# Optimization experiments

Measured on AMD Instinct MI355X. Metric: run time of the kernel, lower is better.

Reference implementation:

```python
import jax, jax.numpy as jnp
import numpy as np
from jax import lax

H = 1024
NH = 16
R = 32
B, S = 32, 1024
LN_EPS = 1e-5

def _gelu(x):
    return jax.nn.gelu(x, approximate=False)

def setup_inputs() -> dict:
    key = jax.random.key(0)
    ks = jax.random.split(key, 24)
    w = lambda k, shape: jax.random.normal(k, shape, jnp.float32) * 0.02
    d = {}
    d['computation_results'] = jax.random.normal(ks[0], (B, S, H), jnp.float32)
    d['max_steps'] = 16
    # rule selector: Linear(H,H), GELU, Linear(H,R)
    d['rule_w1'] = w(ks[1], (H, H)); d['rule_b1'] = jnp.zeros((H,))
    d['rule_w2'] = w(ks[2], (R, H)); d['rule_b2'] = jnp.zeros((R,))
    d['rule_emb'] = jax.random.normal(ks[3], (R, H), jnp.float32)
    # MultiheadAttention packed in-proj [3H,H] and out-proj [H,H]
    d['attn_in_w'] = w(ks[4], (3 * H, H)); d['attn_in_b'] = jnp.zeros((3 * H,))
    d['attn_out_w'] = w(ks[5], (H, H)); d['attn_out_b'] = jnp.zeros((H,))
    # 2-layer LSTM, PyTorch gate order i,f,g,o
    d['lstm_wih0'] = w(ks[6], (4 * H, H)); d['lstm_whh0'] = w(ks[7], (4 * H, H))
    d['lstm_bih0'] = jnp.zeros((4 * H,)); d['lstm_bhh0'] = jnp.zeros((4 * H,))
    d['lstm_wih1'] = w(ks[8], (4 * H, H)); d['lstm_whh1'] = w(ks[9], (4 * H, H))
    d['lstm_bih1'] = jnp.zeros((4 * H,)); d['lstm_bhh1'] = jnp.zeros((4 * H,))
    # step generator: Linear(H,2H), LayerNorm(2H), GELU, Linear(2H,H)
    d['gen_w1'] = w(ks[10], (2 * H, H)); d['gen_b1'] = jnp.zeros((2 * H,))
    d['gen_ln_g'] = jnp.ones((2 * H,)); d['gen_ln_b'] = jnp.zeros((2 * H,))
    d['gen_w2'] = w(ks[11], (H, 2 * H)); d['gen_b2'] = jnp.zeros((H,))
    # step validator: Linear(2H,H), GELU, Linear(H,1), Sigmoid
    d['val_w1'] = w(ks[12], (H, 2 * H)); d['val_b1'] = jnp.zeros((H,))
    d['val_w2'] = w(ks[13], (1, H)); d['val_b2'] = jnp.zeros((1,))
    # proof verifier: Linear(H,H), GELU, Linear(H,1), Sigmoid
    d['ver_w1'] = w(ks[14], (H, H)); d['ver_b1'] = jnp.zeros((H,))
    d['ver_w2'] = w(ks[15], (1, H)); d['ver_b2'] = jnp.zeros((1,))
    return d


def reference(computation_results, max_steps, rule_w1, rule_b1, rule_w2, rule_b2, rule_emb,
              attn_in_w, attn_in_b, attn_out_w, attn_out_b,
              lstm_wih0, lstm_whh0, lstm_bih0, lstm_bhh0,
              lstm_wih1, lstm_whh1, lstm_bih1, lstm_bhh1,
              gen_w1, gen_b1, gen_ln_g, gen_ln_b, gen_w2, gen_b2,
              val_w1, val_b1, val_w2, val_b2,
              ver_w1, ver_b1, ver_w2, ver_b2):
    comp = computation_results
    b, s, h = comp.shape
    dh = h // NH
    scale = dh ** -0.5
    wq, wk, wv = jnp.split(attn_in_w, 3, axis=0)
    bq, bk, bv = jnp.split(attn_in_b, 3, axis=0)
    # K/V projections of the static context, computed once outside the step loop
    K = (comp @ wk.T + bk).reshape(b, s, NH, dh)  # [B,S,NH,dh]
    V = (comp @ wv.T + bv).reshape(b, s, NH, dh)
    lstm_params = ((lstm_wih0, lstm_whh0, lstm_bih0, lstm_bhh0),
                   (lstm_wih1, lstm_whh1, lstm_bih1, lstm_bhh1))

    def step(carry, _):
        ps, hmem, cmem = carry  # ps: [B,H]; hmem/cmem: [2,B,H]
        # rule selection
        logits = _gelu(ps @ rule_w1.T + rule_b1) @ rule_w2.T + rule_b2
        probs = jax.nn.softmax(logits, axis=-1)  # [B,R]
        sel = probs @ rule_emb  # [B,H]
        # single-query multi-head attention over computation context
        q = (ps @ wq.T + bq).reshape(b, NH, dh) * scale
        scores = jnp.einsum('bhd,bshd->bhs', q, K)
        a = jax.nn.softmax(scores, axis=-1)  # [B,NH,S]
        ctx = jnp.einsum('bhs,bshd->bhd', a, V).reshape(b, h) @ attn_out_w.T + attn_out_b
        attn_avg = a.mean(axis=1)  # head-averaged weights, [B,S]
        # 2-layer LSTM cell, one timestep
        x = ps
        hs, cs = [], []
        for l, (wih, whh, bih, bhh) in enumerate(lstm_params):
            g = x @ wih.T + bih + hmem[l] @ whh.T + bhh
            gi, gf, gg, go = jnp.split(g, 4, axis=-1)
            cn = jax.nn.sigmoid(gf) * cmem[l] + jax.nn.sigmoid(gi) * jnp.tanh(gg)
            hn = jax.nn.sigmoid(go) * jnp.tanh(cn)
            hs.append(hn); cs.append(cn); x = hn
        mem_out = x
        # step generator with LayerNorm+GELU
        si = ps + sel + ctx + mem_out
        z = si @ gen_w1.T + gen_b1
        mu = z.mean(axis=-1, keepdims=True)
        var = ((z - mu) ** 2).mean(axis=-1, keepdims=True)
        z = (z - mu) / jnp.sqrt(var + LN_EPS) * gen_ln_g + gen_ln_b
        nxt = _gelu(z) @ gen_w2.T + gen_b2
        val = jax.nn.sigmoid(_gelu(jnp.concatenate([ps, nxt], axis=-1) @ val_w1.T + val_b1) @ val_w2.T + val_b2)
        return (nxt, jnp.stack(hs), jnp.stack(cs)), (nxt, probs, val, attn_avg)

    init_state = comp[:, 0, :]
    carry0 = (init_state, jnp.zeros((2, b, h), comp.dtype), jnp.zeros((2, b, h), comp.dtype))
    (final, _, _), (steps, probs, vals, attn) = lax.scan(step, carry0, None, length=int(max_steps))
    proof_steps = jnp.concatenate([init_state[None], steps], axis=0)  # [T+1,B,H]
    proof_validity = jax.nn.sigmoid(_gelu(final @ ver_w1.T + ver_b1) @ ver_w2.T + ver_b2)  # [B,1]
    return proof_steps, proof_validity, probs, vals, attn
```

## Files before the change

kernel.cpp:

```cpp
#include <hip/hip_runtime.h>

typedef unsigned short u16;
typedef unsigned int u32;
typedef __attribute__((ext_vector_type(8))) short short8v;
typedef __attribute__((ext_vector_type(4))) float f32x4;

#define MFMA16(a,b,c) __builtin_amdgcn_mfma_f32_16x16x32_bf16((a),(b),(c),0,0,0)

__device__ __forceinline__ u16 f2bf(float f){
  u32 u = __float_as_uint(f);
  return (u16)((u + 0x7fffu + ((u >> 16) & 1u)) >> 16);
}
__device__ __forceinline__ float bf2f(u16 h){ return __uint_as_float(((u32)h) << 16); }
__device__ __forceinline__ float gelu_f(float x){ return 0.5f * x * (1.f + erff(x * 0.70710678118654752f)); }
__device__ __forceinline__ float sigm_f(float x){ return 1.f / (1.f + __expf(-x)); }
__device__ __forceinline__ void acc4(float4& a, const float4 b){ a.x+=b.x; a.y+=b.y; a.z+=b.z; a.w+=b.w; }

__device__ __forceinline__ void gl16(const void* g, void* l){
  __builtin_amdgcn_global_load_lds((const __attribute__((address_space(1))) u32*)g,
                                   (__attribute__((address_space(3))) u32*)l, 16, 0, 0);
}

struct CastJobs { const float* s[13]; u16* d[13]; int start[14]; };
__global__ __launch_bounds__(256) void cast_all_k(CastJobs J){
  int bx = blockIdx.x, j = 0;
  #pragma unroll
  for (int t = 0; t < 13; t++) if (bx >= J.start[t + 1]) j = t + 1;
  int i = (bx - J.start[j]) * 1024 + threadIdx.x * 4;
  float4 v = *(const float4*)(J.s[j] + i);
  ushort4 o; o.x = f2bf(v.x); o.y = f2bf(v.y); o.z = f2bf(v.z); o.w = f2bf(v.w);
  *(ushort4*)(J.d[j] + i) = o;
}

__global__ __launch_bounds__(256) void cast_k(const float* __restrict__ s, u16* __restrict__ d, int n){
  int i = (blockIdx.x * 256 + threadIdx.x) * 4;
  if (i + 3 < n){
    float4 v = *(const float4*)(s + i);
    ushort4 o; o.x = f2bf(v.x); o.y = f2bf(v.y); o.z = f2bf(v.z); o.w = f2bf(v.w);
    *(ushort4*)(d + i) = o;
  }
}

__global__ __launch_bounds__(256) void init_k(const float* __restrict__ comp, float* ps0, float* outp,
                                              float* h0, float* c0, float* h1, float* c1){
  int i = blockIdx.x * 256 + threadIdx.x;
  int b = i >> 10, hh = i & 1023;
  float v = comp[(size_t)b * 1048576 + hh];
  ps0[i] = v; outp[i] = v;
  h0[i] = 0.f; c0[i] = 0.f; h1[i] = 0.f; c1[i] = 0.f;
}

__global__ __launch_bounds__(256) void gemmkv_k(const u16* __restrict__ compb,
    const u16* __restrict__ Wk, const u16* __restrict__ Wv,
    const float* __restrict__ bk, const float* __restrict__ bv,
    u16* __restrict__ Kt, u16* __restrict__ Vb)
{
  __shared__ u16 As[128 * 32];
  __shared__ u16 Bs[128 * 32];
  int tid = threadIdx.x;
  const u16 *msrc, *nsrc;
  int m0, n0, isK = (blockIdx.z != 0);
  if (!isK){ m0 = blockIdx.x * 128; n0 = blockIdx.y * 128; msrc = compb; nsrc = Wv; }
  else     { m0 = blockIdx.y * 128; n0 = blockIdx.x * 128; msrc = Wk;    nsrc = compb; }

  int w = tid >> 6, l = tid & 63, lr = l & 15, lk = l >> 4;
  int wm = (w >> 1) * 64, wn = (w & 1) * 64;
  f32x4 acc[4][4];
  #pragma unroll
  for (int i = 0; i < 4; i++)
    #pragma unroll
    for (int j = 0; j < 4; j++) acc[i][j] = (f32x4){0.f,0.f,0.f,0.f};

  int row0 = tid >> 2, k80 = (tid & 3) * 8;
  for (int kc = 0; kc < 1024; kc += 32){
    #pragma unroll
    for (int r = 0; r < 2; r++){
      int i = tid + r * 256;
      int row = row0 + r * 64, k8 = k80;
      gl16(msrc + (size_t)(m0 + row) * 1024 + kc + k8, As + i * 8);
      gl16(nsrc + (size_t)(n0 + row) * 1024 + kc + k8, Bs + i * 8);
    }
    __syncthreads();
    short8v a[4], bb[4];
    #pragma unroll
    for (int mi = 0; mi < 4; mi++) a[mi]  = *(const short8v*)(As + (wm + mi * 16 + lr) * 32 + lk * 8);
    #pragma unroll
    for (int ni = 0; ni < 4; ni++) bb[ni] = *(const short8v*)(Bs + (wn + ni * 16 + lr) * 32 + lk * 8);
    #pragma unroll
    for (int mi = 0; mi < 4; mi++)
      #pragma unroll
      for (int ni = 0; ni < 4; ni++)
        acc[mi][ni] = MFMA16(a[mi], bb[ni], acc[mi][ni]);
    __syncthreads();
  }
  #pragma unroll
  for (int mi = 0; mi < 4; mi++)
    #pragma unroll
    for (int ni = 0; ni < 4; ni++)
      #pragma unroll
      for (int r = 0; r < 4; r++){
        int row = m0 + wm + mi * 16 + lk * 4 + r;
        int col = n0 + wn + ni * 16 + lr;
        if (!isK){
          Vb[(size_t)row * 1024 + col] = f2bf(acc[mi][ni][r] + bv[col]);
        } else {
          int b = col >> 10, s = col & 1023;
          Kt[((size_t)b * 1024 + row) * 1024 + s] = f2bf(acc[mi][ni][r] + bk[row]);
        }
      }
}

struct LinSeg {
  const float* X0; const float* Xa; const float* Xb; const float* Xc;
  const u16* W1; const float* b1;
  const float* Y; const u16* W2; const float* b2;
  float* out; float* out2;
  int K1, ld1, K2, ld2, N, act;
  float scale;
  float* stats;
  const float* lng; const float* lnb; const float* lnstats;
};

__device__ __forceinline__ short8v pack8(float4 v0, float4 v1){
  short8v r;
  r[0]=(short)f2bf(v0.x); r[1]=(short)f2bf(v0.y); r[2]=(short)f2bf(v0.z); r[3]=(short)f2bf(v0.w);
  r[4]=(short)f2bf(v1.x); r[5]=(short)f2bf(v1.y); r[6]=(short)f2bf(v1.z); r[7]=(short)f2bf(v1.w);
  return r;
}

__device__ __forceinline__ short8v load_sum8(const LinSeg& S, int row, int kb){
  size_t o = (size_t)row * S.K1 + kb;
  float4 v0 = *(const float4*)(S.X0 + o);
  float4 v1 = *(const float4*)(S.X0 + o + 4);
  if (S.lng){
    float mu = S.lnstats[row] * (1.f / 2048.f);
    float ms = S.lnstats[32 + row] * (1.f / 2048.f);
    float rstd = rsqrtf(ms - mu * mu + 1e-5f);
    float4 g0 = *(const float4*)(S.lng + kb), g1 = *(const float4*)(S.lng + kb + 4);
    float4 b0 = *(const float4*)(S.lnb + kb), b1 = *(const float4*)(S.lnb + kb + 4);
    v0.x = gelu_f((v0.x - mu) * rstd * g0.x + b0.x);
    v0.y = gelu_f((v0.y - mu) * rstd * g0.y + b0.y);
    v0.z = gelu_f((v0.z - mu) * rstd * g0.z + b0.z);
    v0.w = gelu_f((v0.w - mu) * rstd * g0.w + b0.w);
    v1.x = gelu_f((v1.x - mu) * rstd * g1.x + b1.x);
    v1.y = gelu_f((v1.y - mu) * rstd * g1.y + b1.y);
    v1.z = gelu_f((v1.z - mu) * rstd * g1.z + b1.z);
    v1.w = gelu_f((v1.w - mu) * rstd * g1.w + b1.w);
  } else {
    if (S.Xa){ acc4(v0, *(const float4*)(S.Xa + o)); acc4(v1, *(const float4*)(S.Xa + o + 4)); }
    if (S.Xb){ acc4(v0, *(const float4*)(S.Xb + o)); acc4(v1, *(const float4*)(S.Xb + o + 4)); }
    if (S.Xc){ acc4(v0, *(const float4*)(S.Xc + o)); acc4(v1, *(const float4*)(S.Xc + o + 4)); }
  }
  return pack8(v0, v1);
}
__device__ __forceinline__ short8v load_y8(const float* __restrict__ p){
  return pack8(*(const float4*)(p), *(const float4*)(p + 4));
}

typedef float Red32[32][32];

__device__ void lin_body(const LinSeg& S, int bi, int tid, Red32* red){
  int c0 = bi * 32;
  int w = tid >> 6, l = tid & 63, lr = l & 15, lk = l >> 4;
  f32x4 acc[2][2];
  #pragma unroll
  for (int i = 0; i < 2; i++)
    #pragma unroll
    for (int j = 0; j < 2; j++) acc[i][j] = (f32x4){0.f,0.f,0.f,0.f};

  {
    int chunk = S.K1 >> 3;
    int kb0 = w * chunk + lk * 8;
    for (int kk = 0; kk < chunk; kk += 32){
      int kb = kb0 + kk;
      short8v a0 = load_sum8(S, lr, kb);
      short8v a1 = load_sum8(S, lr + 16, kb);
      short8v w0 = *(const short8v*)(S.W1 + (size_t)(c0 + lr) * S.ld1 + kb);
      short8v w1 = *(const short8v*)(S.W1 + (size_t)(c0 + lr + 16) * S.ld1 + kb);
      acc[0][0] = MFMA16(a0, w0, acc[0][0]);
      acc[0][1] = MFMA16(a0, w1, acc[0][1]);
      acc[1][0] = MFMA16(a1, w0, acc[1][0]);
      acc[1][1] = MFMA16(a1, w1, acc[1][1]);
    }
  }
  if (S.Y){
    int chunk = S.K2 >> 3;
    int kb0 = w * chunk + lk * 8;
    for (int kk = 0; kk < chunk; kk += 32){
      int kb = kb0 + kk;
      short8v a0 = load_y8(S.Y + (size_t)lr * S.K2 + kb);
      short8v a1 = load_y8(S.Y + (size_t)(lr + 16) * S.K2 + kb);
      short8v w0 = *(const short8v*)(S.W2 + (size_t)(c0 + lr) * S.ld2 + kb);
      short8v w1 = *(const short8v*)(S.W2 + (size_t)(c0 + lr + 16) * S.ld2 + kb);
      acc[0][0] = MFMA16(a0, w0, acc[0][0]);
      acc[0][1] = MFMA16(a0, w1, acc[0][1]);
      acc[1][0] = MFMA16(a1, w0, acc[1][0]);
      acc[1][1] = MFMA16(a1, w1, acc[1][1]);
    }
  }
  #pragma unroll
  for (int mi = 0; mi < 2; mi++)
    #pragma unroll
    for (int ni = 0; ni < 2; ni++)
      #pragma unroll
      for (int r = 0; r < 4; r++)
        red[w][mi * 16 + lk * 4 + r][ni * 16 + lr] = acc[mi][ni][r];
  __syncthreads();
  float vout[2]; int iout[2];
  int cnt = 0;
  for (int i = tid; i < 1024; i += 512){
    int row = i >> 5, col = i & 31;
    float v = 0.f;
    #pragma unroll
    for (int ww = 0; ww < 8; ww++) v += red[ww][row][col];
    v += S.b1[c0 + col];
    if (S.b2) v += S.b2[c0 + col];
    if (S.act == 1) v = gelu_f(v);
    else if (S.act == 2) v *= S.scale;
    S.out[(size_t)row * S.N + c0 + col] = v;
    if (S.out2) S.out2[(size_t)row * S.N + c0 + col] = v;
    vout[cnt] = v; iout[cnt] = i; cnt++;
  }
  if (S.stats){
    __syncthreads();
    float* rf = (float*)red;
    rf[iout[0]] = vout[0]; rf[1024 + iout[0]] = vout[0] * vout[0];
    rf[iout[1]] = vout[1]; rf[1024 + iout[1]] = vout[1] * vout[1];
    __syncthreads();
    if (tid < 32){
      float s = 0.f, s2 = 0.f;
      #pragma unroll
      for (int cc = 0; cc < 32; cc++){ s += rf[tid * 32 + cc]; s2 += rf[1024 + tid * 32 + cc]; }
      atomicAdd(S.stats + tid, s);
      atomicAdd(S.stats + 32 + tid, s2);
    }
  }
}

__global__ __launch_bounds__(512) void linmulti_k(LinSeg s0, LinSeg s1, LinSeg s2, int n0, int n1){
  __shared__ float red[8][32][32];
  int bx = blockIdx.x, tid = threadIdx.x;
  if (bx < n0) lin_body(s0, bx, tid, red);
  else if (bx < n0 + n1) lin_body(s1, bx - n0, tid, red);
  else lin_body(s2, bx - n0 - n1, tid, red);
}

__global__ __launch_bounds__(512) void valver_k(const u16* __restrict__ vw1, const float* __restrict__ vb1,
    const u16* __restrict__ verw1, const float* __restrict__ verb1,
    const float* __restrict__ proof, float* __restrict__ v1){
  __shared__ float red[8][32][32];
  int t = blockIdx.y;
  LinSeg S = {};
  if (t < 16){
    S.X0 = proof + (size_t)t * 32768; S.K1 = 1024; S.W1 = vw1; S.ld1 = 2048; S.b1 = vb1;
    S.Y = proof + (size_t)(t + 1) * 32768; S.K2 = 1024; S.W2 = vw1 + 1024; S.ld2 = 2048;
  } else {
    S.X0 = proof + (size_t)16 * 32768; S.K1 = 1024; S.W1 = verw1; S.ld1 = 1024; S.b1 = verb1;
  }
  S.out = v1 + (size_t)t * 32768; S.N = 1024; S.act = 1;
  lin_body(S, blockIdx.x, threadIdx.x, red);
}

__global__ __launch_bounds__(256) void dotsig_b_k(const float* __restrict__ v1,
    const float* __restrict__ w2v, const float* __restrict__ b2v,
    const float* __restrict__ w2ver, const float* __restrict__ b2ver,
    float* __restrict__ out_vals, float* __restrict__ out_valid){
  int t = blockIdx.x;
  const float* w = (t < 16) ? w2v : w2ver;
  const float* bs = (t < 16) ? b2v : b2ver;
  const float* x = v1 + (size_t)t * 32768;
  int b = threadIdx.x >> 3, l8 = threadIdx.x & 7;
  const float* xr = x + (size_t)b * 1024;
  float acc = 0.f;
  #pragma unroll 8
  for (int kk = 0; kk < 32; kk++){
    int k = kk * 32 + l8 * 4;
    float4 xv = *(const float4*)(xr + k);
    float4 wv = *(const float4*)(w + k);
    acc += xv.x * wv.x + xv.y * wv.y + xv.z * wv.z + xv.w * wv.w;
  }
  acc += __shfl_xor(acc, 1); acc += __shfl_xor(acc, 2); acc += __shfl_xor(acc, 4);
  if (l8 == 0){
    float r = sigm_f(acc + bs[0]);
    if (t < 16) out_vals[t * 32 + b] = r; else out_valid[b] = r;
  }
}

__global__ __launch_bounds__(256) void attn_rg0_k(const float* __restrict__ q,
    const u16* __restrict__ Kt, const u16* __restrict__ Vb,
    float* __restrict__ afull, float* __restrict__ ctx0,
    const float* __restrict__ h1a, const float* __restrict__ w2, const float* __restrict__ b2,
    const float* __restrict__ emb, float* __restrict__ probs_out, float* __restrict__ sel,
    const float* __restrict__ g, const float* __restrict__ cprev,
    float* __restrict__ cn, float* __restrict__ hn)
{
  int tid = threadIdx.x;
  if (blockIdx.x >= 544){
    int idx = (blockIdx.x - 544) * 256 + tid;
    int b = idx >> 10, j = idx & 1023;
    const float* gr = g + (size_t)b * 4096;
    float gi = gr[j], gf = gr[1024 + j], gg = gr[2048 + j], go = gr[3072 + j];
    float c = sigm_f(gf) * cprev[idx] + sigm_f(gi) * tanhf(gg);
    cn[idx] = c;
    hn[idx] = sigm_f(go) * tanhf(c);
    return;
  }
  if (blockIdx.x >= 512){
    int b = blockIdx.x - 512;
    __shared__ float lg[32], pshared[32];
    int j = tid >> 3, l8 = tid & 7;
    const float* xr = h1a + b * 1024;
    const float* wr = w2 + j * 1024;
    float acc = 0.f;
    #pragma unroll 8
    for (int kk = 0; kk < 32; kk++){
      int k = kk * 32 + l8 * 4;
      float4 xv = *(const float4*)(xr + k);
      float4 wv = *(const float4*)(wr + k);
      acc += xv.x * wv.x + xv.y * wv.y + xv.z * wv.z + xv.w * wv.w;
    }
    acc += __shfl_xor(acc, 1); acc += __shfl_xor(acc, 2); acc += __shfl_xor(acc, 4);
    if (l8 == 0) lg[j] = acc + b2[j];
    __syncthreads();
    if (tid < 32){
      float v = lg[tid];
      float m = v;
      for (int o = 1; o < 32; o <<= 1) m = fmaxf(m, __shfl_xor(m, o));
      float e = __expf(v - m);
      float s = e;
      for (int o = 1; o < 32; o <<= 1) s += __shfl_xor(s, o);
      float p = e / s;
      pshared[tid] = p;
      probs_out[b * 32 + tid] = p;
    }
    __syncthreads();
    for (int j2 = tid; j2 < 1024; j2 += 256){
      float a2 = 0.f;
      #pragma unroll
      for (int r = 0; r < 32; r++) a2 += pshared[r] * emb[r * 1024 + j2];
      sel[b * 1024 + j2] = a2;
    }
    return;
  }
  int bh = blockIdx.x;
  int b = bh >> 4, h = bh & 15;
  __shared__ float qs[64];
  __shared__ float sc[1024];
  __shared__ float rmx[4], rsm[4];
  __shared__ float ctxp[8][64];
  if (tid < 64) qs[tid] = q[bh * 64 + tid];
  __syncthreads();
  const u32* kt = (const u32*)(Kt + (size_t)bh * 65536);
  float a0 = 0.f, a1 = 0.f, a2 = 0.f, a3 = 0.f;
  #pragma unroll 8
  for (int d = 0; d < 64; d++){
    float qd = qs[d];
    u32 p0 = kt[d * 512 + tid];
    u32 p1 = kt[d * 512 + tid + 256];
    a0 += qd * bf2f((u16)(p0 & 0xffff)); a1 += qd * bf2f((u16)(p0 >> 16));
    a2 += qd * bf2f((u16)(p1 & 0xffff)); a3 += qd * bf2f((u16)(p1 >> 16));
  }
  float mx = fmaxf(fmaxf(a0, a1), fmaxf(a2, a3));
  for (int o = 1; o < 64; o <<= 1) mx = fmaxf(mx, __shfl_xor(mx, o));
  if ((tid & 63) == 0) rmx[tid >> 6] = mx;
  __syncthreads();
  mx = fmaxf(fmaxf(rmx[0], rmx[1]), fmaxf(rmx[2], rmx[3]));
  float e0 = __expf(a0 - mx), e1 = __expf(a1 - mx), e2 = __expf(a2 - mx), e3 = __expf(a3 - mx);
  float sm = e0 + e1 + e2 + e3;
  for (int o = 1; o < 64; o <<= 1) sm += __shfl_xor(sm, o);
  if ((tid & 63) == 0) rsm[tid >> 6] = sm;
  __syncthreads();
  sm = rsm[0] + rsm[1] + rsm[2] + rsm[3];
  float inv = 1.f / sm;
  float* ar = afull + (size_t)bh * 1024;
  float2 w0 = make_float2(e0 * inv, e1 * inv);
  float2 w1 = make_float2(e2 * inv, e3 * inv);
  *(float2*)(sc + 2 * tid) = w0;       *(float2*)(ar + 2 * tid) = w0;
  *(float2*)(sc + 512 + 2 * tid) = w1; *(float2*)(ar + 512 + 2 * tid) = w1;
  __syncthreads();
  int d2 = (tid & 31) * 2, chunk = tid >> 5;
  const u16* vb = Vb + ((size_t)(b * 1024) * 16 + h) * 64 + d2;
  float c0 = 0.f, c1 = 0.f;
  for (int s = chunk * 128; s < chunk * 128 + 128; s++){
    u32 vv = *(const u32*)(vb + (size_t)s * 1024);
    float wv = sc[s];
    c0 += wv * bf2f((u16)(vv & 0xffff));
    c1 += wv * bf2f((u16)(vv >> 16));
  }
  *(float2*)&ctxp[chunk][d2] = make_float2(c0, c1);
  __syncthreads();
  if (tid < 64){
    float r = 0.f;
    #pragma unroll
    for (int c = 0; c < 8; c++) r += ctxp[c][tid];
    ctx0[bh * 64 + tid] = r;
  }
}

__global__ __launch_bounds__(256) void gz_k(const float* __restrict__ g, const float* __restrict__ cprev,
                                            float* __restrict__ cn, float* __restrict__ hn,
                                            float* __restrict__ stats){
  if (blockIdx.x == 0 && threadIdx.x < 64) stats[threadIdx.x] = 0.f;
  int idx = blockIdx.x * 256 + threadIdx.x;
  int b = idx >> 10, j = idx & 1023;
  const float* gr = g + (size_t)b * 4096;
  float gi = gr[j], gf = gr[1024 + j], gg = gr[2048 + j], go = gr[3072 + j];
  float c = sigm_f(gf) * cprev[idx] + sigm_f(gi) * tanhf(gg);
  cn[idx] = c;
  hn[idx] = sigm_f(go) * tanhf(c);
}

__global__ __launch_bounds__(256) void attnavg_all_k(const float* __restrict__ afull, float* __restrict__ out){
  int idx = blockIdx.x * 256 + threadIdx.x;
  int t = idx >> 15, r = idx & 32767;
  int b = r >> 10, s = r & 1023;
  const float* base = afull + (size_t)t * 524288 + (size_t)b * 16384;
  float acc = 0.f;
  #pragma unroll
  for (int h = 0; h < 16; h++) acc += base[h * 1024 + s];
  out[idx] = acc * (1.f / 16.f);
}

extern "C" void kernel_launch(void* const* d_in, const int* in_sizes, int n_in,
                              void* d_out, int out_size, void* d_ws, size_t ws_size,
                              hipStream_t stream) {
  const float* comp      = (const float*)d_in[0];
  const float* rule_w1   = (const float*)d_in[2];
  const float* rule_b1   = (const float*)d_in[3];
  const float* rule_w2   = (const float*)d_in[4];
  const float* rule_b2   = (const float*)d_in[5];
  const float* rule_emb  = (const float*)d_in[6];
  const float* attn_in_w = (const float*)d_in[7];
  const float* attn_in_b = (const float*)d_in[8];
  const float* attn_out_w= (const float*)d_in[9];
  const float* attn_out_b= (const float*)d_in[10];
  const float* wih0 = (const float*)d_in[11];
  const float* whh0 = (const float*)d_in[12];
  const float* bih0 = (const float*)d_in[13];
  const float* bhh0 = (const float*)d_in[14];
  const float* wih1 = (const float*)d_in[15];
  const float* whh1 = (const float*)d_in[16];
  const float* bih1 = (const float*)d_in[17];
  const float* bhh1 = (const float*)d_in[18];
  const float* gen_w1 = (const float*)d_in[19];
  const float* gen_b1 = (const float*)d_in[20];
  const float* ln_g   = (const float*)d_in[21];
  const float* ln_b   = (const float*)d_in[22];
  const float* gen_w2 = (const float*)d_in[23];
  const float* gen_b2 = (const float*)d_in[24];
  const float* val_w1 = (const float*)d_in[25];
  const float* val_b1 = (const float*)d_in[26];
  const float* val_w2 = (const float*)d_in[27];
  const float* val_b2 = (const float*)d_in[28];
  const float* ver_w1 = (const float*)d_in[29];
  const float* ver_b1 = (const float*)d_in[30];
  const float* ver_w2 = (const float*)d_in[31];
  const float* ver_b2 = (const float*)d_in[32];

  float* out_f     = (float*)d_out;
  float* out_proof = out_f;
  float* out_valid = out_f + 17 * 32768;
  float* out_probs = out_valid + 32;
  float* out_vals  = out_probs + 16 * 1024;
  float* out_attn  = out_vals + 16 * 32;

  char* wp = (char*)d_ws;
  auto carve = [&](size_t bytes) -> void* {
    void* p = (void*)wp; wp += (bytes + 255) & ~(size_t)255; return p;
  };
  u16* Kt    = (u16*)carve((size_t)33554432 * 2);
  u16* Vb    = (u16*)carve((size_t)33554432 * 2);
  u16* compb = (u16*)carve((size_t)33554432 * 2);
  float* afull_all = (float*)compb;
  u16* rw1b  = (u16*)carve(2097152);
  u16* wqb   = (u16*)carve(2097152);
  u16* wkb   = (u16*)carve(2097152);
  u16* wvb   = (u16*)carve(2097152);
  u16* aowb  = (u16*)carve(2097152);
  u16* wih0b = (u16*)carve(8388608);
  u16* whh0b = (u16*)carve(8388608);
  u16* wih1b = (u16*)carve(8388608);
  u16* whh1b = (u16*)carve(8388608);
  u16* gw1b  = (u16*)carve(4194304);
  u16* gw2b  = (u16*)carve(4194304);
  u16* vw1b  = (u16*)carve(4194304);
  u16* verw1b= (u16*)carve(2097152);
  float* psb[2]  = { (float*)carve(131072), (float*)carve(131072) };
  float* h0b[2]  = { (float*)carve(131072), (float*)carve(131072) };
  float* c0b[2]  = { (float*)carve(131072), (float*)carve(131072) };
  float* h1b[2]  = { (float*)carve(131072), (float*)carve(131072) };
  float* c1b[2]  = { (float*)carve(131072), (float*)carve(131072) };
  float* h1act = (float*)carve(131072);
  float* sel   = (float*)carve(131072);
  float* qbuf  = (float*)carve(131072);
  float* ctx0  = (float*)carve(131072);
  float* ctxb  = (float*)carve(131072);
  float* gbuf  = (float*)carve(524288);
  float* zbuf  = (float*)carve(262144);
  float* v1buf = (float*)carve(2228224);
  float* lnstats = (float*)carve(256);
  (void)ws_size; (void)in_sizes; (void)n_in; (void)out_size;

  CastJobs J;
  const float* srcs[13] = { rule_w1, attn_in_w, attn_in_w + 1048576, attn_in_w + 2097152,
                            attn_out_w, wih0, whh0, wih1, whh1, gen_w1, gen_w2, val_w1, ver_w1 };
  u16* dsts[13] = { rw1b, wqb, wkb, wvb, aowb, wih0b, whh0b, wih1b, whh1b, gw1b, gw2b, vw1b, verw1b };
  int sizes[13] = { 1048576, 1048576, 1048576, 1048576, 1048576,
                    4194304, 4194304, 4194304, 4194304, 2097152, 2097152, 2097152, 1048576 };
  int st = 0;
  for (int i = 0; i < 13; i++){ J.s[i] = srcs[i]; J.d[i] = dsts[i]; J.start[i] = st; st += sizes[i] / 1024; }
  J.start[13] = st;
  cast_all_k<<<dim3(st), dim3(256), 0, stream>>>(J);
  cast_k<<<dim3(32768), dim3(256), 0, stream>>>(comp, compb, 33554432);

  gemmkv_k<<<dim3(256, 8, 2), dim3(256), 0, stream>>>(compb, wkb, wvb,
      attn_in_b + 1024, attn_in_b + 2048, Kt, Vb);

  init_k<<<dim3(128), dim3(256), 0, stream>>>(comp, psb[0], out_proof,
      h0b[0], c0b[0], h1b[0], c1b[0]);

  auto mkseg = [&](const float* X0, const float* Xa, const float* Xb, const float* Xc,
                   int K1, const u16* W1, int ld1, const float* bb1,
                   const float* Y, int K2, const u16* W2, int ld2, const float* bb2,
                   float* out, int N, int act, float scl, float* out2) -> LinSeg {
    LinSeg S = {};
    S.X0 = X0; S.Xa = Xa; S.Xb = Xb; S.Xc = Xc; S.K1 = K1; S.W1 = W1; S.ld1 = ld1; S.b1 = bb1;
    S.Y = Y; S.K2 = K2; S.W2 = W2; S.ld2 = ld2; S.b2 = bb2;
    S.out = out; S.N = N; S.act = act; S.scale = scl; S.out2 = out2;
    return S;
  };
  auto lin1 = [&](LinSeg S){
    linmulti_k<<<dim3(S.N / 32), dim3(512), 0, stream>>>(S, S, S, S.N / 32, 0);
  };

  for (int t = 0; t < 16; t++){
    int cur = t & 1, nx = cur ^ 1;
    float* ps = psb[cur];
    float* afull_t = afull_all + (size_t)t * 524288;
    LinSeg sRule = mkseg(ps, 0, 0, 0, 1024, rw1b, 1024, rule_b1, 0, 0, 0, 0, 0, h1act, 1024, 1, 0.f, 0);
    LinSeg sQ    = mkseg(ps, 0, 0, 0, 1024, wqb, 1024, attn_in_b, 0, 0, 0, 0, 0, qbuf, 1024, 2, 0.125f, 0);
    LinSeg sL0   = mkseg(ps, 0, 0, 0, 1024, wih0b, 1024, bih0, h0b[cur], 1024, whh0b, 1024, bhh0,
                         gbuf, 4096, 0, 0.f, 0);
    linmulti_k<<<dim3(192), dim3(512), 0, stream>>>(sRule, sQ, sL0, 32, 32);
    attn_rg0_k<<<dim3(672), dim3(256), 0, stream>>>(qbuf, Kt, Vb, afull_t, ctx0,
        h1act, rule_w2, rule_b2, rule_emb, out_probs + t * 1024, sel,
        gbuf, c0b[cur], c0b[nx], h0b[nx]);
    LinSeg sCtx = mkseg(ctx0, 0, 0, 0, 1024, aowb, 1024, attn_out_b, 0, 0, 0, 0, 0, ctxb, 1024, 0, 0.f, 0);
    LinSeg sL1  = mkseg(h0b[nx], 0, 0, 0, 1024, wih1b, 1024, bih1, h1b[cur], 1024, whh1b, 1024, bhh1,
                        gbuf, 4096, 0, 0.f, 0);
    linmulti_k<<<dim3(160), dim3(512), 0, stream>>>(sCtx, sL1, sL1, 32, 128);
    gz_k<<<dim3(128), dim3(256), 0, stream>>>(gbuf, c1b[cur], c1b[nx], h1b[nx], lnstats);
    LinSeg sG1 = mkseg(ps, sel, ctxb, h1b[nx], 1024, gw1b, 1024, gen_b1, 0, 0, 0, 0, 0,
                       zbuf, 2048, 0, 0.f, 0);
    sG1.stats = lnstats;
    lin1(sG1);
    LinSeg sG2 = mkseg(zbuf, 0, 0, 0, 2048, gw2b, 2048, gen_b2, 0, 0, 0, 0, 0,
                       psb[nx], 1024, 0, 0.f, out_proof + (size_t)(t + 1) * 32768);
    sG2.lng = ln_g; sG2.lnb = ln_b; sG2.lnstats = lnstats;
    lin1(sG2);
  }
  valver_k<<<dim3(32, 17), dim3(512), 0, stream>>>(vw1b, val_b1, verw1b, ver_b1, out_proof, v1buf);
  dotsig_b_k<<<dim3(17), dim3(256), 0, stream>>>(v1buf, val_w2, val_b2, ver_w2, ver_b2,
      out_vals, out_valid);
  attnavg_all_k<<<dim3(2048), dim3(256), 0, stream>>>(afull_all, out_attn);
}
```

Measured before the change: 1.948 ms.

## Fuse LSTM cell update into gate GEMM epilogue and tile KV GEMM deeper

Each LSTM gate GEMM block now computes the i,f,g,o columns for 8 hidden units together. The cell and hidden update then runs in the reduction epilogue, which removes the gbuf round trip, the gz_k kernel and the LSTM tail of the attention kernel. The stats zeroing moves into linmulti_k. Separately, the K/V projection GEMM uses a K-chunk of 64 with XOR-swizzled LDS and an XCD-aware block remap for L2 locality. This adds extra per-block reduction work and stride-1024 weight row access in the gate path.

```diff
diff --git a/kernel.cpp b/kernel.cpp
--- a/kernel.cpp
+++ b/kernel.cpp
@@ -55,13 +55,17 @@
     const float* __restrict__ bk, const float* __restrict__ bv,
     u16* __restrict__ Kt, u16* __restrict__ Vb)
 {
-  __shared__ u16 As[128 * 32];
-  __shared__ u16 Bs[128 * 32];
+  __shared__ u16 As[128 * 64];
+  __shared__ u16 Bs[128 * 64];
   int tid = threadIdx.x;
-  const u16 *msrc, *nsrc;
-  int m0, n0, isK = (blockIdx.z != 0);
-  if (!isK){ m0 = blockIdx.x * 128; n0 = blockIdx.y * 128; msrc = compb; nsrc = Wv; }
-  else     { m0 = blockIdx.y * 128; n0 = blockIdx.x * 128; msrc = Wk;    nsrc = compb; }
+  int x = blockIdx.x;
+  int xcd = x & 7, p = x >> 3;
+  int cpanel = xcd * 32 + (p >> 3);
+  int wpanel = p & 7;
+  int isK = (blockIdx.z != 0);
+  const u16 *msrc, *nsrc; int m0, n0;
+  if (!isK){ m0 = cpanel * 128; n0 = wpanel * 128; msrc = compb; nsrc = Wv; }
+  else     { m0 = wpanel * 128; n0 = cpanel * 128; msrc = Wk;    nsrc = compb; }
 
   int w = tid >> 6, l = tid & 63, lr = l & 15, lk = l >> 4;
   int wm = (w >> 1) * 64, wn = (w & 1) * 64;
@@ -71,26 +75,37 @@
     #pragma unroll
     for (int j = 0; j < 4; j++) acc[i][j] = (f32x4){0.f,0.f,0.f,0.f};
 
-  int row0 = tid >> 2, k80 = (tid & 3) * 8;
-  for (int kc = 0; kc < 1024; kc += 32){
-    #pragma unroll
-    for (int r = 0; r < 2; r++){
-      int i = tid + r * 256;
-      int row = row0 + r * 64, k8 = k80;
-      gl16(msrc + (size_t)(m0 + row) * 1024 + kc + k8, As + i * 8);
-      gl16(nsrc + (size_t)(n0 + row) * 1024 + kc + k8, Bs + i * 8);
+  for (int kc = 0; kc < 1024; kc += 64){
+    #pragma unroll
+    for (int r = 0; r < 4; r++){
+      int s = tid + r * 256;
+      int row = s >> 3, pp = s & 7;
+      int lg = pp ^ (row & 7);
+      gl16(msrc + (size_t)(m0 + row) * 1024 + kc + lg * 8, As + s * 8);
+      gl16(nsrc + (size_t)(n0 + row) * 1024 + kc + lg * 8, Bs + s * 8);
     }
     __syncthreads();
-    short8v a[4], bb[4];
-    #pragma unroll
-    for (int mi = 0; mi < 4; mi++) a[mi]  = *(const short8v*)(As + (wm + mi * 16 + lr) * 32 + lk * 8);
-    #pragma unroll
-    for (int ni = 0; ni < 4; ni++) bb[ni] = *(const short8v*)(Bs + (wn + ni * 16 + lr) * 32 + lk * 8);
-    #pragma unroll
-    for (int mi = 0; mi < 4; mi++)
-      #pragma unroll
-      for (int ni = 0; ni < 4; ni++)
-        acc[mi][ni] = MFMA16(a[mi], bb[ni], acc[mi][ni]);
+    #pragma unroll
+    for (int kk = 0; kk < 2; kk++){
+      short8v a[4], bb[4];
+      #pragma unroll
+      for (int mi = 0; mi < 4; mi++){
+        int row = wm + mi * 16 + lr;
+        int ph = (kk * 4 + lk) ^ (row & 7);
+        a[mi] = *(const short8v*)(As + row * 64 + ph * 8);
+      }
+      #pragma unroll
+      for (int ni = 0; ni < 4; ni++){
+        int row = wn + ni * 16 + lr;
+        int ph = (kk * 4 + lk) ^ (row & 7);
+        bb[ni] = *(const short8v*)(Bs + row * 64 + ph * 8);
+      }
+      #pragma unroll
+      for (int mi = 0; mi < 4; mi++)
+        #pragma unroll
+        for (int ni = 0; ni < 4; ni++)
+          acc[mi][ni] = MFMA16(a[mi], bb[ni], acc[mi][ni]);
+    }
     __syncthreads();
   }
   #pragma unroll
@@ -115,10 +130,11 @@
   const u16* W1; const float* b1;
   const float* Y; const u16* W2; const float* b2;
   float* out; float* out2;
-  int K1, ld1, K2, ld2, N, act;
+  int K1, ld1, K2, ld2, N, act, gate;
   float scale;
   float* stats;
   const float* lng; const float* lnb; const float* lnstats;
+  const float* cprev; float* cout; float* hout;
 };
 
 __device__ __forceinline__ short8v pack8(float4 v0, float4 v1){
@@ -160,8 +176,10 @@
 typedef float Red32[32][32];
 
 __device__ void lin_body(const LinSeg& S, int bi, int tid, Red32* red){
-  int c0 = bi * 32;
+  int c0 = bi * 32, j0 = bi * 8;
   int w = tid >> 6, l = tid & 63, lr = l & 15, lk = l >> 4;
+  int wc0 = S.gate ? ((lr >> 3) << 10) + j0 + (lr & 7) : c0 + lr;
+  int wc1 = S.gate ? (((lr + 16) >> 3) << 10) + j0 + ((lr + 16) & 7) : c0 + lr + 16;
   f32x4 acc[2][2];
   #pragma unroll
   for (int i = 0; i < 2; i++)
@@ -175,8 +193,8 @@
       int kb = kb0 + kk;
       short8v a0 = load_sum8(S, lr, kb);
       short8v a1 = load_sum8(S, lr + 16, kb);
-      short8v w0 = *(const short8v*)(S.W1 + (size_t)(c0 + lr) * S.ld1 + kb);
-      short8v w1 = *(const short8v*)(S.W1 + (size_t)(c0 + lr + 16) * S.ld1 + kb);
+      short8v w0 = *(const short8v*)(S.W1 + (size_t)wc0 * S.ld1 + kb);
+      short8v w1 = *(const short8v*)(S.W1 + (size_t)wc1 * S.ld1 + kb);
       acc[0][0] = MFMA16(a0, w0, acc[0][0]);
       acc[0][1] = MFMA16(a0, w1, acc[0][1]);
       acc[1][0] = MFMA16(a1, w0, acc[1][0]);
@@ -190,8 +208,8 @@
       int kb = kb0 + kk;
       short8v a0 = load_y8(S.Y + (size_t)lr * S.K2 + kb);
       short8v a1 = load_y8(S.Y + (size_t)(lr + 16) * S.K2 + kb);
-      short8v w0 = *(const short8v*)(S.W2 + (size_t)(c0 + lr) * S.ld2 + kb);
-      short8v w1 = *(const short8v*)(S.W2 + (size_t)(c0 + lr + 16) * S.ld2 + kb);
+      short8v w0 = *(const short8v*)(S.W2 + (size_t)wc0 * S.ld2 + kb);
+      short8v w1 = *(const short8v*)(S.W2 + (size_t)wc1 * S.ld2 + kb);
       acc[0][0] = MFMA16(a0, w0, acc[0][0]);
       acc[0][1] = MFMA16(a0, w1, acc[0][1]);
       acc[1][0] = MFMA16(a1, w0, acc[1][0]);
@@ -206,6 +224,29 @@
       for (int r = 0; r < 4; r++)
         red[w][mi * 16 + lk * 4 + r][ni * 16 + lr] = acc[mi][ni][r];
   __syncthreads();
+  if (S.gate){
+    if (tid < 256){
+      int row = tid >> 3, j = tid & 7;
+      float s[4];
+      #pragma unroll
+      for (int g = 0; g < 4; g++){
+        float v = 0.f;
+        #pragma unroll
+        for (int ww = 0; ww < 8; ww++) v += red[ww][row][g * 8 + j];
+        s[g] = v;
+      }
+      int gc = j0 + j;
+      float gI = s[0] + S.b1[gc]        + S.b2[gc];
+      float gF = s[1] + S.b1[1024 + gc] + S.b2[1024 + gc];
+      float gG = s[2] + S.b1[2048 + gc] + S.b2[2048 + gc];
+      float gO = s[3] + S.b1[3072 + gc] + S.b2[3072 + gc];
+      int idx = row * 1024 + gc;
+      float cN = sigm_f(gF) * S.cprev[idx] + sigm_f(gI) * tanhf(gG);
+      S.cout[idx] = cN;
+      S.hout[idx] = sigm_f(gO) * tanhf(cN);
+    }
+    return;
+  }
   float vout[2]; int iout[2];
   int cnt = 0;
   for (int i = tid; i < 1024; i += 512){
@@ -237,9 +278,11 @@
   }
 }
 
-__global__ __launch_bounds__(512) void linmulti_k(LinSeg s0, LinSeg s1, LinSeg s2, int n0, int n1){
+__global__ __launch_bounds__(512) void linmulti_k(LinSeg s0, LinSeg s1, LinSeg s2, int n0, int n1,
+                                                  float* zero64){
   __shared__ float red[8][32][32];
   int bx = blockIdx.x, tid = threadIdx.x;
+  if (zero64 && bx == 0 && tid < 64) zero64[tid] = 0.f;
   if (bx < n0) lin_body(s0, bx, tid, red);
   else if (bx < n0 + n1) lin_body(s1, bx - n0, tid, red);
   else lin_body(s2, bx - n0 - n1, tid, red);
@@ -286,25 +329,13 @@
   }
 }
 
-__global__ __launch_bounds__(256) void attn_rg0_k(const float* __restrict__ q,
+__global__ __launch_bounds__(256) void attn_r2_k(const float* __restrict__ q,
     const u16* __restrict__ Kt, const u16* __restrict__ Vb,
     float* __restrict__ afull, float* __restrict__ ctx0,
     const float* __restrict__ h1a, const float* __restrict__ w2, const float* __restrict__ b2,
-    const float* __restrict__ emb, float* __restrict__ probs_out, float* __restrict__ sel,
-    const float* __restrict__ g, const float* __restrict__ cprev,
-    float* __restrict__ cn, float* __restrict__ hn)
+    const float* __restrict__ emb, float* __restrict__ probs_out, float* __restrict__ sel)
 {
   int tid = threadIdx.x;
-  if (blockIdx.x >= 544){
-    int idx = (blockIdx.x - 544) * 256 + tid;
-    int b = idx >> 10, j = idx & 1023;
-    const float* gr = g + (size_t)b * 4096;
-    float gi = gr[j], gf = gr[1024 + j], gg = gr[2048 + j], go = gr[3072 + j];
-    float c = sigm_f(gf) * cprev[idx] + sigm_f(gi) * tanhf(gg);
-    cn[idx] = c;
-    hn[idx] = sigm_f(go) * tanhf(c);
-    return;
-  }
   if (blockIdx.x >= 512){
     int b = blockIdx.x - 512;
     __shared__ float lg[32], pshared[32];
@@ -395,19 +426,6 @@
     for (int c = 0; c < 8; c++) r += ctxp[c][tid];
     ctx0[bh * 64 + tid] = r;
   }
-}
-
-__global__ __launch_bounds__(256) void gz_k(const float* __restrict__ g, const float* __restrict__ cprev,
-                                            float* __restrict__ cn, float* __restrict__ hn,
-                                            float* __restrict__ stats){
-  if (blockIdx.x == 0 && threadIdx.x < 64) stats[threadIdx.x] = 0.f;
-  int idx = blockIdx.x * 256 + threadIdx.x;
-  int b = idx >> 10, j = idx & 1023;
-  const float* gr = g + (size_t)b * 4096;
-  float gi = gr[j], gf = gr[1024 + j], gg = gr[2048 + j], go = gr[3072 + j];
-  float c = sigm_f(gf) * cprev[idx] + sigm_f(gi) * tanhf(gg);
-  cn[idx] = c;
-  hn[idx] = sigm_f(go) * tanhf(c);
 }
 
 __global__ __launch_bounds__(256) void attnavg_all_k(const float* __restrict__ afull, float* __restrict__ out){
@@ -495,7 +513,6 @@
   float* qbuf  = (float*)carve(131072);
   float* ctx0  = (float*)carve(131072);
   float* ctxb  = (float*)carve(131072);
-  float* gbuf  = (float*)carve(524288);
   float* zbuf  = (float*)carve(262144);
   float* v1buf = (float*)carve(2228224);
   float* lnstats = (float*)carve(256);
@@ -513,7 +530,7 @@
   cast_all_k<<<dim3(st), dim3(256), 0, stream>>>(J);
   cast_k<<<dim3(32768), dim3(256), 0, stream>>>(comp, compb, 33554432);
 
-  gemmkv_k<<<dim3(256, 8, 2), dim3(256), 0, stream>>>(compb, wkb, wvb,
+  gemmkv_k<<<dim3(2048, 1, 2), dim3(256), 0, stream>>>(compb, wkb, wvb,
       attn_in_b + 1024, attn_in_b + 2048, Kt, Vb);
 
   init_k<<<dim3(128), dim3(256), 0, stream>>>(comp, psb[0], out_proof,
@@ -530,7 +547,7 @@
     return S;
   };
   auto lin1 = [&](LinSeg S){
-    linmulti_k<<<dim3(S.N / 32), dim3(512), 0, stream>>>(S, S, S, S.N / 32, 0);
+    linmulti_k<<<dim3(S.N / 32), dim3(512), 0, stream>>>(S, S, S, S.N / 32, 0, nullptr);
   };
 
   for (int t = 0; t < 16; t++){
@@ -540,16 +557,16 @@
     LinSeg sRule = mkseg(ps, 0, 0, 0, 1024, rw1b, 1024, rule_b1, 0, 0, 0, 0, 0, h1act, 1024, 1, 0.f, 0);
     LinSeg sQ    = mkseg(ps, 0, 0, 0, 1024, wqb, 1024, attn_in_b, 0, 0, 0, 0, 0, qbuf, 1024, 2, 0.125f, 0);
     LinSeg sL0   = mkseg(ps, 0, 0, 0, 1024, wih0b, 1024, bih0, h0b[cur], 1024, whh0b, 1024, bhh0,
-                         gbuf, 4096, 0, 0.f, 0);
-    linmulti_k<<<dim3(192), dim3(512), 0, stream>>>(sRule, sQ, sL0, 32, 32);
-    attn_rg0_k<<<dim3(672), dim3(256), 0, stream>>>(qbuf, Kt, Vb, afull_t, ctx0,
-        h1act, rule_w2, rule_b2, rule_emb, out_probs + t * 1024, sel,
-        gbuf, c0b[cur], c0b[nx], h0b[nx]);
+                         0, 4096, 0, 0.f, 0);
+    sL0.gate = 1; sL0.cprev = c0b[cur]; sL0.cout = c0b[nx]; sL0.hout = h0b[nx];
+    linmulti_k<<<dim3(192), dim3(512), 0, stream>>>(sRule, sQ, sL0, 32, 32, nullptr);
+    attn_r2_k<<<dim3(544), dim3(256), 0, stream>>>(qbuf, Kt, Vb, afull_t, ctx0,
+        h1act, rule_w2, rule_b2, rule_emb, out_probs + t * 1024, sel);
     LinSeg sCtx = mkseg(ctx0, 0, 0, 0, 1024, aowb, 1024, attn_out_b, 0, 0, 0, 0, 0, ctxb, 1024, 0, 0.f, 0);
     LinSeg sL1  = mkseg(h0b[nx], 0, 0, 0, 1024, wih1b, 1024, bih1, h1b[cur], 1024, whh1b, 1024, bhh1,
-                        gbuf, 4096, 0, 0.f, 0);
-    linmulti_k<<<dim3(160), dim3(512), 0, stream>>>(sCtx, sL1, sL1, 32, 128);
-    gz_k<<<dim3(128), dim3(256), 0, stream>>>(gbuf, c1b[cur], c1b[nx], h1b[nx], lnstats);
+                        0, 4096, 0, 0.f, 0);
+    sL1.gate = 1; sL1.cprev = c1b[cur]; sL1.cout = c1b[nx]; sL1.hout = h1b[nx];
+    linmulti_k<<<dim3(160), dim3(512), 0, stream>>>(sCtx, sL1, sL1, 32, 128, lnstats);
     LinSeg sG1 = mkseg(ps, sel, ctxb, h1b[nx], 1024, gw1b, 1024, gen_b1, 0, 0, 0, 0, 0,
                        zbuf, 2048, 0, 0.f, 0);
     sG1.stats = lnstats;
```

Measured after the change: 1.925 ms. Within noise of the previous version (-1.2%).
